# Performance work log

Measured on AMD Instinct MI355X. Metric: run time of the kernel, lower is better.

## Reference

```python
import jax, jax.numpy as jnp
import numpy as np

B, N, D = 8, 192, 768   # batch of docs, events per doc, embed_dim
H = 150                 # Score hidden_dim
PAD = -1000.0           # pad_and_stack fill value


def setup_inputs() -> dict:
    key = jax.random.key(0)
    ks = jax.random.split(key, 7)
    s1 = 1.0 / np.sqrt(3 * D)
    s2 = 1.0 / np.sqrt(H)
    return {
        "event_embed": jax.random.normal(ks[0], (B, N, D), jnp.float32),
        "W1": jax.random.normal(ks[1], (3 * D, H), jnp.float32) * s1,
        "b1": jnp.zeros((H,), jnp.float32),
        "W2": jax.random.normal(ks[2], (H, H), jnp.float32) * s2,
        "b2": jnp.zeros((H,), jnp.float32),
        "W3": jax.random.normal(ks[3], (H, 1), jnp.float32) * s2,
        "b3": jnp.zeros((1,), jnp.float32),
    }


def reference(event_embed, W1, b1, W2, b2, W3, b3):
    Bq, Nq, Dq = event_embed.shape
    # antecedent pairs: for each event i, all k < i (row-major, matches torch loop order)
    rows, cols = jnp.tril_indices(Nq, k=-1)          # [P], P = N*(N-1)/2
    i_g = event_embed[:, rows]                        # [B, P, D]
    j_g = event_embed[:, cols]                        # [B, P, D]
    pairs = jnp.concatenate([i_g, j_g, i_g * j_g], axis=-1)  # [B, P, 3D]
    # Score MLP (dropout is identity at inference)
    h = jax.nn.relu(pairs @ W1 + b1)                  # [B, P, H]
    h = jax.nn.relu(h @ W2 + b2)                      # [B, P, H]
    s = (h @ W3 + b3)[..., 0]                         # [B, P]
    # Scatter pair scores into [B, N, N]; diagonal stays 0 = epsilon score.
    logits = jnp.zeros((Bq, Nq, Nq), event_embed.dtype).at[:, rows, cols].set(s)
    tri = jnp.tril(jnp.ones((Nq, Nq), dtype=bool))    # valid cols: k <= i (incl epsilon)
    masked = jnp.where(tri, logits, -jnp.inf)
    probs = jax.nn.softmax(masked, axis=-1)           # ragged softmax per event row
    return jnp.where(tri, probs, jnp.asarray(PAD, probs.dtype))  # pad_and_stack(value=-1000)
```

## Files before the change

kernel.cpp:

```cpp
#include <hip/hip_runtime.h>
#include <hip/hip_bf16.h>

#define NSEQ   192
#define PADV   -1000.0f
#define NEGINF -1.0e30f

typedef __bf16 bf16x8 __attribute__((ext_vector_type(8)));
typedef float  f32x4  __attribute__((ext_vector_type(4)));

__device__ __forceinline__ void glds16(const void* g, void* l) {
  __builtin_amdgcn_global_load_lds(
      (const __attribute__((address_space(1))) unsigned int*)g,
      (__attribute__((address_space(3))) unsigned int*)l, 16, 0, 0);
}

#define MFMA16(a, b, c) __builtin_amdgcn_mfma_f32_16x16x32_bf16((a), (b), (c), 0, 0, 0)

__global__ __launch_bounds__(256) void prep_pack(const float* __restrict__ W1,
                                                 const float* __restrict__ W2,
                                                 __bf16* __restrict__ W1abp,
                                                 __bf16* __restrict__ W1cp,
                                                 __bf16* __restrict__ W2p) {
  int idx = blockIdx.x * 256 + threadIdx.x;
  if (idx < 245760) {
    int e = idx & 7, l = (idx >> 3) & 63, t = idx >> 9;
    int ct = t % 20, kk = t / 20;
    int k = kk * 32 + ((l >> 4) << 3) + e;
    int hp = ct * 16 + (l & 15);
    int col = (hp < 160) ? hp : hp - 160;
    int rbase = (hp < 160) ? 0 : 768;
    float v = (col < 150) ? W1[(size_t)(rbase + k) * 150 + col] : 0.f;
    W1abp[idx] = (__bf16)v;
  } else if (idx < 245760 + 122880) {
    int j = idx - 245760;
    int e = j & 7, l = (j >> 3) & 63, t = j >> 9;
    int ct = t % 10, kk = t / 10;
    int k = kk * 32 + ((l >> 4) << 3) + e;
    int h = ct * 16 + (l & 15);
    float v = (h < 150) ? W1[(size_t)(1536 + k) * 150 + h] : 0.f;
    W1cp[j] = (__bf16)v;
  } else {
    int j = idx - 368640;
    int e = j & 7, l = (j >> 3) & 63, t = j >> 9;
    int ct = t % 10, kk = t / 10;
    int k = kk * 32 + ((l >> 4) << 3) + e;
    int h = ct * 16 + (l & 15);
    float v = (k < 150 && h < 150) ? W2[(size_t)k * 150 + h] : 0.f;
    W2p[j] = (__bf16)v;
  }
}

__global__ __launch_bounds__(256) void prep_gemm(const float* __restrict__ E,
                                                 const __bf16* __restrict__ W1abp,
                                                 float* __restrict__ A12) {
  int tid = threadIdx.x;
  int w = tid >> 6, l = tid & 63, m = l & 15, kg = l >> 4;
  int mt = blockIdx.x >> 3;
  int c  = blockIdx.x & 7;
  const float* ep = E + (size_t)(mt * 16 + m) * 768 + c * 96;

  f32x4 acc[5];
#pragma unroll
  for (int u = 0; u < 5; ++u) acc[u] = (f32x4){0.f, 0.f, 0.f, 0.f};

#pragma unroll
  for (int kk = 0; kk < 3; ++kk) {
    int k = kk * 32 + kg * 8;
    f32x4 x0 = *(const f32x4*)(ep + k);
    f32x4 x1 = *(const f32x4*)(ep + k + 4);
    bf16x8 af;
#pragma unroll
    for (int e = 0; e < 4; ++e) { af[e] = (__bf16)x0[e]; af[e + 4] = (__bf16)x1[e]; }
    const bf16x8* wp = (const bf16x8*)W1abp + (size_t)(((c * 3 + kk) * 20) + w * 5) * 64 + l;
#pragma unroll
    for (int u = 0; u < 5; ++u)
      acc[u] = MFMA16(af, wp[u * 64], acc[u]);
  }
#pragma unroll
  for (int u = 0; u < 5; ++u)
#pragma unroll
    for (int r = 0; r < 4; ++r)
      atomicAdd(&A12[(size_t)(mt * 16 + kg * 4 + r) * 320 + (w * 5 + u) * 16 + m], acc[u][r]);
}

__global__ __launch_bounds__(256, 2) void pair_mlp(
    const float* __restrict__ E, const float* __restrict__ A12,
    const __bf16* __restrict__ W1cp, const __bf16* __restrict__ W2p,
    const float* __restrict__ b1, const float* __restrict__ b2,
    const float* __restrict__ W3, const float* __restrict__ b3,
    float* __restrict__ out) {
  __shared__ alignas(16) char pool[72704];
  __bf16* Wb  = (__bf16*)pool;
  __bf16* h1s = (__bf16*)(pool + 51200);

  const int tid = threadIdx.x;
  const int w = tid >> 6, l = tid & 63;
  const int m = l & 15, kg = l >> 4;

  int blk = blockIdx.x;
  int b = blk / 156, r0 = blk - b * 156;
  int it = (int)((sqrtf(4.f * (float)r0 + 1.f) - 1.f) * 0.5f);
  while (it * it + it > r0) --it;
  while ((it + 1) * (it + 1) + (it + 1) <= r0) ++it;
  int jt = r0 - it * it - it;

  const int ibase = b * NSEQ + it * 16;
  const int jrow0 = b * NSEQ + jt * 8 + w * 2;

  f32x4 acc[2][10];
#pragma unroll
  for (int rg = 0; rg < 2; ++rg) {
    const float* a2p = A12 + (size_t)(jrow0 + rg) * 320 + 160;
#pragma unroll
    for (int ct = 0; ct < 10; ++ct) {
      int h = ct * 16 + m;
      float base2 = a2p[h] + ((h < 150) ? b1[h] : 0.f);
#pragma unroll
      for (int rr = 0; rr < 4; ++rr)
        acc[rg][ct][rr] = A12[(size_t)(ibase + kg * 4 + rr) * 320 + h] + base2;
    }
  }

  const float* eibase = E + (size_t)(ibase + m) * 768;
  const float* ejb0   = E + (size_t)jrow0 * 768;
  const float* ejb1   = E + (size_t)(jrow0 + 1) * 768;

#pragma unroll
  for (int q = 0; q < 5; ++q)
    glds16(W1cp + (size_t)(w * 5 + q) * 512 + l * 8, Wb + (w * 5 + q) * 512);
  f32x4 eic[4], ejc[2][4], ein[4], ejn[2][4];
#pragma unroll
  for (int q = 0; q < 4; ++q) {
    int off = (q >> 1) * 32 + kg * 8 + (q & 1) * 4;
    eic[q]    = *(const f32x4*)(eibase + off);
    ejc[0][q] = *(const f32x4*)(ejb0 + off);
    ejc[1][q] = *(const f32x4*)(ejb1 + off);
  }

  for (int t = 0; t < 12; ++t) {
    int tn = (t < 11) ? t + 1 : 11;
    int bn = (t + 1) & 1;
#pragma unroll
    for (int q = 0; q < 5; ++q)
      glds16(W1cp + ((size_t)tn * 20 + w * 5 + q) * 512 + l * 8,
             Wb + (bn * 20 + w * 5 + q) * 512);
#pragma unroll
    for (int q = 0; q < 4; ++q) {
      int off = tn * 64 + (q >> 1) * 32 + kg * 8 + (q & 1) * 4;
      ein[q]    = *(const f32x4*)(eibase + off);
      ejn[0][q] = *(const f32x4*)(ejb0 + off);
      ejn[1][q] = *(const f32x4*)(ejb1 + off);
    }
    asm volatile("s_waitcnt vmcnt(17)" ::: "memory");
    __builtin_amdgcn_s_barrier();

    const __bf16* wb = Wb + (t & 1) * 10240;
#pragma unroll
    for (int s = 0; s < 2; ++s) {
      bf16x8 af0, af1;
#pragma unroll
      for (int e = 0; e < 4; ++e) {
        af0[e]     = (__bf16)(eic[2 * s][e]     * ejc[0][2 * s][e]);
        af0[e + 4] = (__bf16)(eic[2 * s + 1][e] * ejc[0][2 * s + 1][e]);
        af1[e]     = (__bf16)(eic[2 * s][e]     * ejc[1][2 * s][e]);
        af1[e + 4] = (__bf16)(eic[2 * s + 1][e] * ejc[1][2 * s + 1][e]);
      }
#pragma unroll
      for (int ct = 0; ct < 10; ++ct) {
        bf16x8 wf = *(const bf16x8*)(wb + (s * 10 + ct) * 512 + l * 8);
        acc[0][ct] = MFMA16(af0, wf, acc[0][ct]);
        acc[1][ct] = MFMA16(af1, wf, acc[1][ct]);
      }
    }
    __builtin_amdgcn_s_barrier();
#pragma unroll
    for (int q = 0; q < 4; ++q) {
      eic[q] = ein[q]; ejc[0][q] = ejn[0][q]; ejc[1][q] = ejn[1][q];
    }
  }

#pragma unroll
  for (int rr = 0; rr < 4; ++rr)
#pragma unroll
    for (int ct = 0; ct < 10; ++ct)
      h1s[(w * 16 + kg * 4 + rr) * 168 + ct * 16 + m] =
          (__bf16)fmaxf(acc[0][ct][rr], 0.f);

  for (int f = w; f < 50; f += 4)
    glds16(W2p + (size_t)f * 512 + l * 8, Wb + f * 512);
  __syncthreads();

  float b3v = b3[0];
#pragma unroll
  for (int rg = 0; rg < 2; ++rg) {
    if (rg == 1) {
#pragma unroll
      for (int rr = 0; rr < 4; ++rr)
#pragma unroll
        for (int ct = 0; ct < 10; ++ct)
          h1s[(w * 16 + kg * 4 + rr) * 168 + ct * 16 + m] =
              (__bf16)fmaxf(acc[1][ct][rr], 0.f);
    }
    f32x4 acc2[10];
#pragma unroll
    for (int u = 0; u < 10; ++u) acc2[u] = (f32x4){0.f, 0.f, 0.f, 0.f};
#pragma unroll
    for (int s = 0; s < 5; ++s) {
      bf16x8 a2f = *(const bf16x8*)&h1s[(w * 16 + m) * 168 + s * 32 + kg * 8];
#pragma unroll
      for (int ct = 0; ct < 10; ++ct) {
        bf16x8 wf = *(const bf16x8*)(Wb + (s * 10 + ct) * 512 + l * 8);
        acc2[ct] = MFMA16(a2f, wf, acc2[ct]);
      }
    }
    float part[4] = {0.f, 0.f, 0.f, 0.f};
#pragma unroll
    for (int ct = 0; ct < 10; ++ct) {
      int h = ct * 16 + m;
      float bb = (h < 150) ? b2[h] : 0.f;
      float w3 = (h < 150) ? W3[h] : 0.f;
#pragma unroll
      for (int rr = 0; rr < 4; ++rr)
        part[rr] += fmaxf(acc2[ct][rr] + bb, 0.f) * w3;
    }
#pragma unroll
    for (int off = 8; off >= 1; off >>= 1) {
#pragma unroll
      for (int rr = 0; rr < 4; ++rr) part[rr] += __shfl_xor(part[rr], off, 16);
    }
#pragma unroll
    for (int rr = 0; rr < 4; ++rr) {
      if (m == rr) {
        int il = it * 16 + kg * 4 + rr;
        int jl = jt * 8 + w * 2 + rg;
        if (jl < il)
          out[((size_t)(b * NSEQ + il)) * NSEQ + jl] = part[rr] + b3v;
      }
    }
  }
}

__global__ __launch_bounds__(256) void softmax_rows(float* __restrict__ out) {
  int w = threadIdx.x >> 6, l = threadIdx.x & 63;
  int blk = blockIdx.x * 4 + w;
  int i = blk % NSEQ;
  size_t base = (size_t)blk * NSEQ;
  float v[3];
  float mx = NEGINF;
#pragma unroll
  for (int t = 0; t < 3; ++t) {
    int j = l + 64 * t;
    float x = (j < i) ? out[base + j] : (j == i ? 0.f : NEGINF);
    v[t] = x;
    mx = fmaxf(mx, x);
  }
#pragma unroll
  for (int off = 32; off >= 1; off >>= 1) mx = fmaxf(mx, __shfl_xor(mx, off, 64));
  float s = 0.f;
#pragma unroll
  for (int t = 0; t < 3; ++t) s += __expf(v[t] - mx);
#pragma unroll
  for (int off = 32; off >= 1; off >>= 1) s += __shfl_xor(s, off, 64);
  float inv = 1.0f / s;
#pragma unroll
  for (int t = 0; t < 3; ++t) {
    int j = l + 64 * t;
    out[base + j] = (j <= i) ? __expf(v[t] - mx) * inv : PADV;
  }
}

extern "C" void kernel_launch(void* const* d_in, const int* in_sizes, int n_in,
                              void* d_out, int out_size, void* d_ws, size_t ws_size,
                              hipStream_t stream) {
  const float* E  = (const float*)d_in[0];
  const float* W1 = (const float*)d_in[1];
  const float* b1 = (const float*)d_in[2];
  const float* W2 = (const float*)d_in[3];
  const float* b2 = (const float*)d_in[4];
  const float* W3 = (const float*)d_in[5];
  const float* b3 = (const float*)d_in[6];
  float* out = (float*)d_out;

  char* ws = (char*)d_ws;
  float*  A12   = (float*)(ws);
  __bf16* W1abp = (__bf16*)(ws + 1966080);
  __bf16* W1cp  = (__bf16*)(ws + 2457600);
  __bf16* W2p   = (__bf16*)(ws + 2703360);

  hipMemsetAsync(A12, 0, 1966080, stream);
  prep_pack<<<1540, 256, 0, stream>>>(W1, W2, W1abp, W1cp, W2p);
  prep_gemm<<<768, 256, 0, stream>>>(E, W1abp, A12);
  pair_mlp<<<1248, 256, 0, stream>>>(E, A12, W1cp, W2p, b1, b2, W3, b3, out);
  softmax_rows<<<384, 256, 0, stream>>>(out);
}
```

Before: 109.7 us.

## Stage event rows in LDS as bf16 and double-buffer W2 in pair MLP

Instead of streaming fp32 event rows from global memory into registers on every K step, the kernel now converts the 16 i-rows and 8 j-rows to bf16 once into swizzled shared memory and reads them from there in the inner loop. The W1c loop now waits only on the weight prefetch and keeps a double-buffered pipeline. Layer 2 computes both row groups together from two separate h1 buffers, with W2 streamed in double-buffered chunks. This cuts redundant global loads and register pressure, but shared memory grows to about 76KB, which may limit occupancy to two blocks per CU. Rounding e_i and e_j to bf16 before the multiply adds extra precision loss.

```diff
diff --git a/kernel.cpp b/kernel.cpp
--- a/kernel.cpp
+++ b/kernel.cpp
@@ -89,9 +89,13 @@
     const float* __restrict__ b1, const float* __restrict__ b2,
     const float* __restrict__ W3, const float* __restrict__ b3,
     float* __restrict__ out) {
-  __shared__ alignas(16) char pool[72704];
-  __bf16* Wb  = (__bf16*)pool;
-  __bf16* h1s = (__bf16*)(pool + 51200);
+  __shared__ alignas(16) char pool[77824];
+  __bf16* Wb   = (__bf16*)pool;
+  char*   eib  = pool + 40960;
+  char*   ejb  = pool + 65536;
+  __bf16* W2b  = (__bf16*)pool;
+  __bf16* h1r1 = (__bf16*)(pool + 20480);
+  __bf16* h1r0 = (__bf16*)(pool + 40960);
 
   const int tid = threadIdx.x;
   const int w = tid >> 6, l = tid & 63;
@@ -105,12 +109,45 @@
   int jt = r0 - it * it - it;
 
   const int ibase = b * NSEQ + it * 16;
-  const int jrow0 = b * NSEQ + jt * 8 + w * 2;
+  const int jbase = b * NSEQ + jt * 8;
+
+#pragma unroll
+  for (int q = 0; q < 5; ++q)
+    glds16(W1cp + (size_t)(w * 5 + q) * 512 + l * 8, Wb + (w * 5 + q) * 512);
+
+  {
+    int r = tid >> 4, c0 = tid & 15;
+    const float* src = E + (size_t)(ibase + r) * 768;
+#pragma unroll
+    for (int p = 0; p < 6; ++p) {
+      int c = c0 + 16 * p;
+      int kf = ((c * 16) ^ ((r & 7) << 4)) >> 2;
+      f32x4 a = *(const f32x4*)(src + kf);
+      f32x4 bq = *(const f32x4*)(src + kf + 4);
+      bf16x8 v;
+#pragma unroll
+      for (int e = 0; e < 4; ++e) { v[e] = (__bf16)a[e]; v[e + 4] = (__bf16)bq[e]; }
+      *(bf16x8*)(eib + r * 1536 + c * 16) = v;
+    }
+    int r2 = tid >> 5, c02 = tid & 31;
+    const float* src2 = E + (size_t)(jbase + r2) * 768;
+#pragma unroll
+    for (int p = 0; p < 3; ++p) {
+      int c = c02 + 32 * p;
+      const float* sp = src2 + c * 8;
+      f32x4 a = *(const f32x4*)(sp);
+      f32x4 bq = *(const f32x4*)(sp + 4);
+      bf16x8 v;
+#pragma unroll
+      for (int e = 0; e < 4; ++e) { v[e] = (__bf16)a[e]; v[e + 4] = (__bf16)bq[e]; }
+      *(bf16x8*)(ejb + r2 * 1536 + c * 16) = v;
+    }
+  }
 
   f32x4 acc[2][10];
 #pragma unroll
   for (int rg = 0; rg < 2; ++rg) {
-    const float* a2p = A12 + (size_t)(jrow0 + rg) * 320 + 160;
+    const float* a2p = A12 + (size_t)(jbase + w * 2 + rg) * 320 + 160;
 #pragma unroll
     for (int ct = 0; ct < 10; ++ct) {
       int h = ct * 16 + m;
@@ -121,49 +158,23 @@
     }
   }
 
-  const float* eibase = E + (size_t)(ibase + m) * 768;
-  const float* ejb0   = E + (size_t)jrow0 * 768;
-  const float* ejb1   = E + (size_t)(jrow0 + 1) * 768;
-
-#pragma unroll
-  for (int q = 0; q < 5; ++q)
-    glds16(W1cp + (size_t)(w * 5 + q) * 512 + l * 8, Wb + (w * 5 + q) * 512);
-  f32x4 eic[4], ejc[2][4], ein[4], ejn[2][4];
-#pragma unroll
-  for (int q = 0; q < 4; ++q) {
-    int off = (q >> 1) * 32 + kg * 8 + (q & 1) * 4;
-    eic[q]    = *(const f32x4*)(eibase + off);
-    ejc[0][q] = *(const f32x4*)(ejb0 + off);
-    ejc[1][q] = *(const f32x4*)(ejb1 + off);
-  }
-
-  for (int t = 0; t < 12; ++t) {
-    int tn = (t < 11) ? t + 1 : 11;
-    int bn = (t + 1) & 1;
-#pragma unroll
-    for (int q = 0; q < 5; ++q)
-      glds16(W1cp + ((size_t)tn * 20 + w * 5 + q) * 512 + l * 8,
-             Wb + (bn * 20 + w * 5 + q) * 512);
-#pragma unroll
-    for (int q = 0; q < 4; ++q) {
-      int off = tn * 64 + (q >> 1) * 32 + kg * 8 + (q & 1) * 4;
-      ein[q]    = *(const f32x4*)(eibase + off);
-      ejn[0][q] = *(const f32x4*)(ejb0 + off);
-      ejn[1][q] = *(const f32x4*)(ejb1 + off);
-    }
-    asm volatile("s_waitcnt vmcnt(17)" ::: "memory");
-    __builtin_amdgcn_s_barrier();
-
+  asm volatile("s_waitcnt vmcnt(0)" ::: "memory");
+  __syncthreads();
+
+  auto compute = [&](int t) {
     const __bf16* wb = Wb + (t & 1) * 10240;
 #pragma unroll
     for (int s = 0; s < 2; ++s) {
+      int jb = t * 128 + s * 64 + kg * 16;
+      bf16x8 eiv = *(const bf16x8*)(eib + m * 1536 + (jb ^ ((m & 7) << 4)));
+      bf16x8 ej0 = *(const bf16x8*)(ejb + (w * 2) * 1536 + jb);
+      bf16x8 ej1 = *(const bf16x8*)(ejb + (w * 2 + 1) * 1536 + jb);
       bf16x8 af0, af1;
 #pragma unroll
-      for (int e = 0; e < 4; ++e) {
-        af0[e]     = (__bf16)(eic[2 * s][e]     * ejc[0][2 * s][e]);
-        af0[e + 4] = (__bf16)(eic[2 * s + 1][e] * ejc[0][2 * s + 1][e]);
-        af1[e]     = (__bf16)(eic[2 * s][e]     * ejc[1][2 * s][e]);
-        af1[e + 4] = (__bf16)(eic[2 * s + 1][e] * ejc[1][2 * s + 1][e]);
+      for (int e = 0; e < 8; ++e) {
+        float ei = (float)eiv[e];
+        af0[e] = (__bf16)(ei * (float)ej0[e]);
+        af1[e] = (__bf16)(ei * (float)ej1[e]);
       }
 #pragma unroll
       for (int ct = 0; ct < 10; ++ct) {
@@ -172,47 +183,61 @@
         acc[1][ct] = MFMA16(af1, wf, acc[1][ct]);
       }
     }
-    __builtin_amdgcn_s_barrier();
-#pragma unroll
-    for (int q = 0; q < 4; ++q) {
-      eic[q] = ein[q]; ejc[0][q] = ejn[0][q]; ejc[1][q] = ejn[1][q];
-    }
-  }
+  };
+
+  for (int t = 0; t < 11; ++t) {
+#pragma unroll
+    for (int q = 0; q < 5; ++q)
+      glds16(W1cp + ((size_t)(t + 1) * 20 + w * 5 + q) * 512 + l * 8,
+             Wb + (((t + 1) & 1) * 20 + w * 5 + q) * 512);
+    asm volatile("s_waitcnt vmcnt(5)\ns_barrier" ::: "memory");
+    compute(t);
+    asm volatile("s_barrier" ::: "memory");
+  }
+  asm volatile("s_waitcnt vmcnt(0)\ns_barrier" ::: "memory");
+  compute(11);
+  asm volatile("s_barrier" ::: "memory");
 
 #pragma unroll
   for (int rr = 0; rr < 4; ++rr)
 #pragma unroll
-    for (int ct = 0; ct < 10; ++ct)
-      h1s[(w * 16 + kg * 4 + rr) * 168 + ct * 16 + m] =
+    for (int ct = 0; ct < 10; ++ct) {
+      h1r0[(w * 16 + kg * 4 + rr) * 168 + ct * 16 + m] =
           (__bf16)fmaxf(acc[0][ct][rr], 0.f);
-
-  for (int f = w; f < 50; f += 4)
-    glds16(W2p + (size_t)f * 512 + l * 8, Wb + f * 512);
+      h1r1[(w * 16 + kg * 4 + rr) * 160 + ct * 16 + m] =
+          (__bf16)fmaxf(acc[1][ct][rr], 0.f);
+    }
+
+  for (int f = w; f < 10; f += 4)
+    glds16(W2p + (size_t)f * 512 + l * 8, W2b + f * 512);
+  asm volatile("s_waitcnt vmcnt(0)" ::: "memory");
   __syncthreads();
 
+  f32x4 acc2[2][10];
+#pragma unroll
+  for (int rg = 0; rg < 2; ++rg)
+#pragma unroll
+    for (int u = 0; u < 10; ++u) acc2[rg][u] = (f32x4){0.f, 0.f, 0.f, 0.f};
+
+  for (int s = 0; s < 5; ++s) {
+    if (s < 4)
+      for (int f = w; f < 10; f += 4)
+        glds16(W2p + (size_t)((s + 1) * 10 + f) * 512 + l * 8,
+               W2b + ((s + 1) & 1) * 5120 + f * 512);
+    bf16x8 a0 = *(const bf16x8*)(h1r0 + (w * 16 + m) * 168 + s * 32 + kg * 8);
+    bf16x8 a1 = *(const bf16x8*)(h1r1 + (w * 16 + m) * 160 + s * 32 + kg * 8);
+#pragma unroll
+    for (int ct = 0; ct < 10; ++ct) {
+      bf16x8 wf = *(const bf16x8*)(W2b + (s & 1) * 5120 + ct * 512 + l * 8);
+      acc2[0][ct] = MFMA16(a0, wf, acc2[0][ct]);
+      acc2[1][ct] = MFMA16(a1, wf, acc2[1][ct]);
+    }
+    asm volatile("s_waitcnt vmcnt(0)\ns_barrier" ::: "memory");
+  }
+
   float b3v = b3[0];
 #pragma unroll
   for (int rg = 0; rg < 2; ++rg) {
-    if (rg == 1) {
-#pragma unroll
-      for (int rr = 0; rr < 4; ++rr)
-#pragma unroll
-        for (int ct = 0; ct < 10; ++ct)
-          h1s[(w * 16 + kg * 4 + rr) * 168 + ct * 16 + m] =
-              (__bf16)fmaxf(acc[1][ct][rr], 0.f);
-    }
-    f32x4 acc2[10];
-#pragma unroll
-    for (int u = 0; u < 10; ++u) acc2[u] = (f32x4){0.f, 0.f, 0.f, 0.f};
-#pragma unroll
-    for (int s = 0; s < 5; ++s) {
-      bf16x8 a2f = *(const bf16x8*)&h1s[(w * 16 + m) * 168 + s * 32 + kg * 8];
-#pragma unroll
-      for (int ct = 0; ct < 10; ++ct) {
-        bf16x8 wf = *(const bf16x8*)(Wb + (s * 10 + ct) * 512 + l * 8);
-        acc2[ct] = MFMA16(a2f, wf, acc2[ct]);
-      }
-    }
     float part[4] = {0.f, 0.f, 0.f, 0.f};
 #pragma unroll
     for (int ct = 0; ct < 10; ++ct) {
@@ -221,7 +246,7 @@
       float w3 = (h < 150) ? W3[h] : 0.f;
 #pragma unroll
       for (int rr = 0; rr < 4; ++rr)
-        part[rr] += fmaxf(acc2[ct][rr] + bb, 0.f) * w3;
+        part[rr] += fmaxf(acc2[rg][ct][rr] + bb, 0.f) * w3;
     }
 #pragma unroll
     for (int off = 8; off >= 1; off >>= 1) {
```

Measured after the change: 88.43 us. 19.4% less time.

## Retile pair MLP to 16x16 pair tiles with LDS-staged bf16 embeddings

Applied to the files above, without the earlier changes.

The pair_mlp kernel now handles 16x16 (i,j) tiles instead of 16x8, which halves the block count. Both embedding row sets are staged once into swizzled LDS as bf16, replacing per-iteration global fp32 loads. Weights for layers 1 and 2 are streamed through a smaller double-buffered LDS ring with s_setprio around the MFMA bursts, and blocks are interleaved across batches. This trades a larger accumulator register footprint (40 f32x4) and more barriers for fewer redundant global reads of E and W1c.

```diff
diff --git a/kernel.cpp b/kernel.cpp
--- a/kernel.cpp
+++ b/kernel.cpp
@@ -31,21 +31,21 @@
     int rbase = (hp < 160) ? 0 : 768;
     float v = (col < 150) ? W1[(size_t)(rbase + k) * 150 + col] : 0.f;
     W1abp[idx] = (__bf16)v;
-  } else if (idx < 245760 + 122880) {
+  } else if (idx < 393216) {
     int j = idx - 245760;
-    int e = j & 7, l = (j >> 3) & 63, t = j >> 9;
-    int ct = t % 10, kk = t / 10;
+    int kk = j / 6144, rem = j % 6144;
+    int q = rem >> 9, l = (rem >> 3) & 63, e = rem & 7;
     int k = kk * 32 + ((l >> 4) << 3) + e;
-    int h = ct * 16 + (l & 15);
-    float v = (h < 150) ? W1[(size_t)(1536 + k) * 150 + h] : 0.f;
+    int h = q * 16 + (l & 15);
+    float v = (q < 10 && h < 150) ? W1[(size_t)(1536 + k) * 150 + h] : 0.f;
     W1cp[j] = (__bf16)v;
   } else {
-    int j = idx - 368640;
-    int e = j & 7, l = (j >> 3) & 63, t = j >> 9;
-    int ct = t % 10, kk = t / 10;
-    int k = kk * 32 + ((l >> 4) << 3) + e;
-    int h = ct * 16 + (l & 15);
-    float v = (k < 150 && h < 150) ? W2[(size_t)k * 150 + h] : 0.f;
+    int j = idx - 393216;
+    int s = j / 6144, rem = j % 6144;
+    int q = rem >> 9, l = (rem >> 3) & 63, e = rem & 7;
+    int k = s * 32 + ((l >> 4) << 3) + e;
+    int h = q * 16 + (l & 15);
+    float v = (q < 10 && k < 150 && h < 150) ? W2[(size_t)k * 150 + h] : 0.f;
     W2p[j] = (__bf16)v;
   }
 }
@@ -89,154 +89,206 @@
     const float* __restrict__ b1, const float* __restrict__ b2,
     const float* __restrict__ W3, const float* __restrict__ b3,
     float* __restrict__ out) {
-  __shared__ alignas(16) char pool[72704];
+  __shared__ alignas(16) char pool[73728];
   __bf16* Wb  = (__bf16*)pool;
-  __bf16* h1s = (__bf16*)(pool + 51200);
+  char*   eib = pool + 24576;
+  char*   ejb = pool + 49152;
+  char*   h1b = pool + 24576;
 
   const int tid = threadIdx.x;
   const int w = tid >> 6, l = tid & 63;
   const int m = l & 15, kg = l >> 4;
 
-  int blk = blockIdx.x;
-  int b = blk / 156, r0 = blk - b * 156;
-  int it = (int)((sqrtf(4.f * (float)r0 + 1.f) - 1.f) * 0.5f);
-  while (it * it + it > r0) --it;
-  while ((it + 1) * (it + 1) + (it + 1) <= r0) ++it;
-  int jt = r0 - it * it - it;
+  int bid = blockIdx.x;
+  int blk = (bid & 7) * 78 + (bid >> 3);
+  int b = blk / 78, r0 = blk - b * 78;
+  int it = (int)((sqrtf(8.f * (float)r0 + 1.f) - 1.f) * 0.5f);
+  while (it * (it + 1) / 2 > r0) --it;
+  while ((it + 1) * (it + 2) / 2 <= r0) ++it;
+  int jt = r0 - it * (it + 1) / 2;
 
   const int ibase = b * NSEQ + it * 16;
-  const int jrow0 = b * NSEQ + jt * 8 + w * 2;
-
-  f32x4 acc[2][10];
-#pragma unroll
-  for (int rg = 0; rg < 2; ++rg) {
-    const float* a2p = A12 + (size_t)(jrow0 + rg) * 320 + 160;
+  const int jbase = b * NSEQ + jt * 16;
+
+#pragma unroll
+  for (int q = 0; q < 3; ++q)
+    glds16(W1cp + (size_t)(w * 3 + q) * 512 + l * 8, Wb + (w * 3 + q) * 512);
+
+  {
+    int r = tid >> 4, c0 = tid & 15;
+    const float* si = E + (size_t)(ibase + r) * 768;
+    const float* sj = E + (size_t)(jbase + r) * 768;
+#pragma unroll
+    for (int p = 0; p < 6; ++p) {
+      int c = c0 + 16 * p;
+      int cs = c ^ (r & 7);
+      f32x4 a0 = *(const f32x4*)(si + cs * 8);
+      f32x4 a1 = *(const f32x4*)(si + cs * 8 + 4);
+      f32x4 b0 = *(const f32x4*)(sj + cs * 8);
+      f32x4 b1q = *(const f32x4*)(sj + cs * 8 + 4);
+      bf16x8 vi, vj;
+#pragma unroll
+      for (int e = 0; e < 4; ++e) {
+        vi[e] = (__bf16)a0[e]; vi[e + 4] = (__bf16)a1[e];
+        vj[e] = (__bf16)b0[e]; vj[e + 4] = (__bf16)b1q[e];
+      }
+      *(bf16x8*)(eib + r * 1536 + c * 16) = vi;
+      *(bf16x8*)(ejb + r * 1536 + c * 16) = vj;
+    }
+  }
+
+  f32x4 acc1[10][4];
+#pragma unroll
+  for (int ct = 0; ct < 10; ++ct) {
+    f32x4 a1v = *(const f32x4*)(A12 + (size_t)(ibase + m) * 320 + ct * 16 + kg * 4);
+    f32x4 b1v;
+#pragma unroll
+    for (int r = 0; r < 4; ++r) {
+      int h = ct * 16 + kg * 4 + r;
+      b1v[r] = (h < 150) ? b1[h] : 0.f;
+    }
+#pragma unroll
+    for (int pt = 0; pt < 4; ++pt) {
+      f32x4 a2v = *(const f32x4*)(A12 + (size_t)(jbase + w * 4 + pt) * 320 + 160 + ct * 16 + kg * 4);
+#pragma unroll
+      for (int r = 0; r < 4; ++r) acc1[ct][pt][r] = a1v[r] + a2v[r] + b1v[r];
+    }
+  }
+
+  __syncthreads();
+
+  for (int kk = 0; kk < 24; ++kk) {
+    if (kk < 23) {
+#pragma unroll
+      for (int q = 0; q < 3; ++q)
+        glds16(W1cp + ((size_t)(kk + 1) * 12 + w * 3 + q) * 512 + l * 8,
+               Wb + (((kk + 1) & 1) * 12 + w * 3 + q) * 512);
+      asm volatile("s_waitcnt vmcnt(3)" ::: "memory");
+    } else {
+      asm volatile("s_waitcnt vmcnt(0)" ::: "memory");
+    }
+    __builtin_amdgcn_s_barrier();
+
+    const __bf16* wbuf = Wb + (kk & 1) * 6144;
+    int cbase = kk * 4 + kg;
+    bf16x8 eiv = *(const bf16x8*)(eib + m * 1536 + (cbase ^ (m & 7)) * 16);
+    float eif[8];
+#pragma unroll
+    for (int e = 0; e < 8; ++e) eif[e] = (float)eiv[e];
+    bf16x8 pf[4];
+#pragma unroll
+    for (int pt = 0; pt < 4; ++pt) {
+      int jr = w * 4 + pt;
+      bf16x8 ejv = *(const bf16x8*)(ejb + jr * 1536 + (cbase ^ (jr & 7)) * 16);
+#pragma unroll
+      for (int e = 0; e < 8; ++e)
+        pf[pt][e] = (__bf16)(eif[e] * (float)ejv[e]);
+    }
+    __builtin_amdgcn_s_setprio(1);
 #pragma unroll
     for (int ct = 0; ct < 10; ++ct) {
-      int h = ct * 16 + m;
-      float base2 = a2p[h] + ((h < 150) ? b1[h] : 0.f);
-#pragma unroll
-      for (int rr = 0; rr < 4; ++rr)
-        acc[rg][ct][rr] = A12[(size_t)(ibase + kg * 4 + rr) * 320 + h] + base2;
-    }
-  }
-
-  const float* eibase = E + (size_t)(ibase + m) * 768;
-  const float* ejb0   = E + (size_t)jrow0 * 768;
-  const float* ejb1   = E + (size_t)(jrow0 + 1) * 768;
-
-#pragma unroll
-  for (int q = 0; q < 5; ++q)
-    glds16(W1cp + (size_t)(w * 5 + q) * 512 + l * 8, Wb + (w * 5 + q) * 512);
-  f32x4 eic[4], ejc[2][4], ein[4], ejn[2][4];
-#pragma unroll
-  for (int q = 0; q < 4; ++q) {
-    int off = (q >> 1) * 32 + kg * 8 + (q & 1) * 4;
-    eic[q]    = *(const f32x4*)(eibase + off);
-    ejc[0][q] = *(const f32x4*)(ejb0 + off);
-    ejc[1][q] = *(const f32x4*)(ejb1 + off);
-  }
-
-  for (int t = 0; t < 12; ++t) {
-    int tn = (t < 11) ? t + 1 : 11;
-    int bn = (t + 1) & 1;
-#pragma unroll
-    for (int q = 0; q < 5; ++q)
-      glds16(W1cp + ((size_t)tn * 20 + w * 5 + q) * 512 + l * 8,
-             Wb + (bn * 20 + w * 5 + q) * 512);
-#pragma unroll
-    for (int q = 0; q < 4; ++q) {
-      int off = tn * 64 + (q >> 1) * 32 + kg * 8 + (q & 1) * 4;
-      ein[q]    = *(const f32x4*)(eibase + off);
-      ejn[0][q] = *(const f32x4*)(ejb0 + off);
-      ejn[1][q] = *(const f32x4*)(ejb1 + off);
-    }
-    asm volatile("s_waitcnt vmcnt(17)" ::: "memory");
+      bf16x8 wf = *(const bf16x8*)(wbuf + ct * 512 + l * 8);
+#pragma unroll
+      for (int pt = 0; pt < 4; ++pt)
+        acc1[ct][pt] = MFMA16(wf, pf[pt], acc1[ct][pt]);
+    }
+    __builtin_amdgcn_s_setprio(0);
     __builtin_amdgcn_s_barrier();
-
-    const __bf16* wb = Wb + (t & 1) * 10240;
-#pragma unroll
-    for (int s = 0; s < 2; ++s) {
-      bf16x8 af0, af1;
-#pragma unroll
-      for (int e = 0; e < 4; ++e) {
-        af0[e]     = (__bf16)(eic[2 * s][e]     * ejc[0][2 * s][e]);
-        af0[e + 4] = (__bf16)(eic[2 * s + 1][e] * ejc[0][2 * s + 1][e]);
-        af1[e]     = (__bf16)(eic[2 * s][e]     * ejc[1][2 * s][e]);
-        af1[e + 4] = (__bf16)(eic[2 * s + 1][e] * ejc[1][2 * s + 1][e]);
+  }
+
+  auto write_h1 = [&](int ptL, int pt) {
+    char* hb = h1b + w * 10752 + ptL * 5376 + m * 336;
+#pragma unroll
+    for (int ct = 0; ct < 10; ++ct) {
+      union { __bf16 h[4]; unsigned u[2]; } cv;
+      cv.h[0] = (__bf16)fmaxf(acc1[ct][pt][0], 0.f);
+      cv.h[1] = (__bf16)fmaxf(acc1[ct][pt][1], 0.f);
+      cv.h[2] = (__bf16)fmaxf(acc1[ct][pt][2], 0.f);
+      cv.h[3] = (__bf16)fmaxf(acc1[ct][pt][3], 0.f);
+      *(unsigned*)(hb + ct * 32 + kg * 8)     = cv.u[0];
+      *(unsigned*)(hb + ct * 32 + kg * 8 + 4) = cv.u[1];
+    }
+  };
+  write_h1(0, 0);
+  write_h1(1, 1);
+
+  float w3v[10], b2v[10];
+#pragma unroll
+  for (int ct = 0; ct < 10; ++ct) {
+    int h = ct * 16 + m;
+    w3v[ct] = (h < 150) ? W3[h] : 0.f;
+    b2v[ct] = (h < 150) ? b2[h] : 0.f;
+  }
+  float b3v = b3[0];
+
+#pragma unroll
+  for (int q = 0; q < 3; ++q)
+    glds16(W2p + (size_t)(w * 3 + q) * 512 + l * 8, Wb + (w * 3 + q) * 512);
+
+  f32x4 acc2[10][2];
+#pragma unroll
+  for (int ct = 0; ct < 10; ++ct) {
+    acc2[ct][0] = (f32x4){0.f, 0.f, 0.f, 0.f};
+    acc2[ct][1] = (f32x4){0.f, 0.f, 0.f, 0.f};
+  }
+
+  for (int skk = 0; skk < 10; ++skk) {
+    int s = (skk >= 5) ? skk - 5 : skk;
+    if (skk == 5) { write_h1(0, 2); write_h1(1, 3); }
+    if (skk < 9) {
+      int n = skk + 1;
+      int sl = (n >= 5) ? n - 5 : n;
+#pragma unroll
+      for (int q = 0; q < 3; ++q)
+        glds16(W2p + ((size_t)sl * 12 + w * 3 + q) * 512 + l * 8,
+               Wb + ((n & 1) * 12 + w * 3 + q) * 512);
+      asm volatile("s_waitcnt vmcnt(3)" ::: "memory");
+    } else {
+      asm volatile("s_waitcnt vmcnt(0)" ::: "memory");
+    }
+    __builtin_amdgcn_s_barrier();
+
+    const __bf16* wbuf = Wb + (skk & 1) * 6144;
+    bf16x8 af0 = *(const bf16x8*)(h1b + w * 10752 +        m * 336 + s * 64 + kg * 16);
+    bf16x8 af1 = *(const bf16x8*)(h1b + w * 10752 + 5376 + m * 336 + s * 64 + kg * 16);
+    __builtin_amdgcn_s_setprio(1);
+#pragma unroll
+    for (int ct = 0; ct < 10; ++ct) {
+      bf16x8 wf = *(const bf16x8*)(wbuf + ct * 512 + l * 8);
+      acc2[ct][0] = MFMA16(af0, wf, acc2[ct][0]);
+      acc2[ct][1] = MFMA16(af1, wf, acc2[ct][1]);
+    }
+    __builtin_amdgcn_s_setprio(0);
+
+    if (s == 4) {
+      int pass = skk / 5;
+#pragma unroll
+      for (int ptL = 0; ptL < 2; ++ptL) {
+        float part[4] = {0.f, 0.f, 0.f, 0.f};
+#pragma unroll
+        for (int ct = 0; ct < 10; ++ct)
+#pragma unroll
+          for (int r = 0; r < 4; ++r)
+            part[r] += fmaxf(acc2[ct][ptL][r] + b2v[ct], 0.f) * w3v[ct];
+#pragma unroll
+        for (int off = 8; off >= 1; off >>= 1)
+#pragma unroll
+          for (int r = 0; r < 4; ++r) part[r] += __shfl_xor(part[r], off, 16);
+        int jl = jt * 16 + w * 4 + pass * 2 + ptL;
+#pragma unroll
+        for (int r = 0; r < 4; ++r) {
+          if (m == r) {
+            int il = it * 16 + kg * 4 + r;
+            if (jl < il)
+              out[(size_t)(b * NSEQ + il) * NSEQ + jl] = part[r] + b3v;
+          }
+        }
+#pragma unroll
+        for (int ct = 0; ct < 10; ++ct)
+          acc2[ct][ptL] = (f32x4){0.f, 0.f, 0.f, 0.f};
       }
-#pragma unroll
-      for (int ct = 0; ct < 10; ++ct) {
-        bf16x8 wf = *(const bf16x8*)(wb + (s * 10 + ct) * 512 + l * 8);
-        acc[0][ct] = MFMA16(af0, wf, acc[0][ct]);
-        acc[1][ct] = MFMA16(af1, wf, acc[1][ct]);
-      }
     }
     __builtin_amdgcn_s_barrier();
-#pragma unroll
-    for (int q = 0; q < 4; ++q) {
-      eic[q] = ein[q]; ejc[0][q] = ejn[0][q]; ejc[1][q] = ejn[1][q];
-    }
-  }
-
-#pragma unroll
-  for (int rr = 0; rr < 4; ++rr)
-#pragma unroll
-    for (int ct = 0; ct < 10; ++ct)
-      h1s[(w * 16 + kg * 4 + rr) * 168 + ct * 16 + m] =
-          (__bf16)fmaxf(acc[0][ct][rr], 0.f);
-
-  for (int f = w; f < 50; f += 4)
-    glds16(W2p + (size_t)f * 512 + l * 8, Wb + f * 512);
-  __syncthreads();
-
-  float b3v = b3[0];
-#pragma unroll
-  for (int rg = 0; rg < 2; ++rg) {
-    if (rg == 1) {
-#pragma unroll
-      for (int rr = 0; rr < 4; ++rr)
-#pragma unroll
-        for (int ct = 0; ct < 10; ++ct)
-          h1s[(w * 16 + kg * 4 + rr) * 168 + ct * 16 + m] =
-              (__bf16)fmaxf(acc[1][ct][rr], 0.f);
-    }
-    f32x4 acc2[10];
-#pragma unroll
-    for (int u = 0; u < 10; ++u) acc2[u] = (f32x4){0.f, 0.f, 0.f, 0.f};
-#pragma unroll
-    for (int s = 0; s < 5; ++s) {
-      bf16x8 a2f = *(const bf16x8*)&h1s[(w * 16 + m) * 168 + s * 32 + kg * 8];
-#pragma unroll
-      for (int ct = 0; ct < 10; ++ct) {
-        bf16x8 wf = *(const bf16x8*)(Wb + (s * 10 + ct) * 512 + l * 8);
-        acc2[ct] = MFMA16(a2f, wf, acc2[ct]);
-      }
-    }
-    float part[4] = {0.f, 0.f, 0.f, 0.f};
-#pragma unroll
-    for (int ct = 0; ct < 10; ++ct) {
-      int h = ct * 16 + m;
-      float bb = (h < 150) ? b2[h] : 0.f;
-      float w3 = (h < 150) ? W3[h] : 0.f;
-#pragma unroll
-      for (int rr = 0; rr < 4; ++rr)
-        part[rr] += fmaxf(acc2[ct][rr] + bb, 0.f) * w3;
-    }
-#pragma unroll
-    for (int off = 8; off >= 1; off >>= 1) {
-#pragma unroll
-      for (int rr = 0; rr < 4; ++rr) part[rr] += __shfl_xor(part[rr], off, 16);
-    }
-#pragma unroll
-    for (int rr = 0; rr < 4; ++rr) {
-      if (m == rr) {
-        int il = it * 16 + kg * 4 + rr;
-        int jl = jt * 8 + w * 2 + rg;
-        if (jl < il)
-          out[((size_t)(b * NSEQ + il)) * NSEQ + jl] = part[rr] + b3v;
-      }
-    }
   }
 }
 
@@ -285,11 +337,11 @@
   float*  A12   = (float*)(ws);
   __bf16* W1abp = (__bf16*)(ws + 1966080);
   __bf16* W1cp  = (__bf16*)(ws + 2457600);
-  __bf16* W2p   = (__bf16*)(ws + 2703360);
+  __bf16* W2p   = (__bf16*)(ws + 2752512);
 
   hipMemsetAsync(A12, 0, 1966080, stream);
-  prep_pack<<<1540, 256, 0, stream>>>(W1, W2, W1abp, W1cp, W2p);
+  prep_pack<<<1656, 256, 0, stream>>>(W1, W2, W1abp, W1cp, W2p);
   prep_gemm<<<768, 256, 0, stream>>>(E, W1abp, A12);
-  pair_mlp<<<1248, 256, 0, stream>>>(E, A12, W1cp, W2p, b1, b2, W3, b3, out);
+  pair_mlp<<<624, 256, 0, stream>>>(E, A12, W1cp, W2p, b1, b2, W3, b3, out);
   softmax_rows<<<384, 256, 0, stream>>>(out);
 }
```

Result: faster. 100.4 us (-8.4%).
